# Performance work log

Hardware: AMD Instinct MI355X
Metric: run time of the kernel (lower is better)

## Reference

```python
import jax, jax.numpy as jnp
import numpy as np

UNITS = 1000


def gru_step(x, h, W, U, b):
    # Keras GRU, reset_after=True. b: [2, 3*units] = (input bias, recurrent bias)
    gx = x @ W + b[0]
    gh = h @ U + b[1]
    xz, xr, xh = jnp.split(gx, 3, axis=-1)
    hz, hr, hh_ = jnp.split(gh, 3, axis=-1)
    z = jax.nn.sigmoid(xz + hz)
    r = jax.nn.sigmoid(xr + hr)
    hh = jnp.tanh(xh + r * hh_)
    return z * h + (1.0 - z) * hh


def setup_inputs() -> dict:
    key = jax.random.key(0)
    ks = jax.random.split(key, 12)
    V1, E, U = 32001, 100, UNITS
    B, S = 64, 25
    sc = 0.05
    return {
        "x": jax.random.randint(ks[0], (B, S), 0, V1, dtype=jnp.int32),
        "target": jax.random.randint(ks[1], (B, S), 0, V1, dtype=jnp.int32),
        "start_token": 2,
        "emb_table": jax.random.normal(ks[2], (V1, E), jnp.float32) * sc,
        "enc_kernel": jax.random.normal(ks[3], (E, 3 * U), jnp.float32) * sc,
        "enc_recurrent": jax.random.normal(ks[4], (U, 3 * U), jnp.float32) * sc,
        "enc_bias": jax.random.normal(ks[5], (2, 3 * U), jnp.float32) * sc,
        "dec_kernel": jax.random.normal(ks[6], (E, 3 * U), jnp.float32) * sc,
        "dec_recurrent": jax.random.normal(ks[7], (U, 3 * U), jnp.float32) * sc,
        "dec_bias": jax.random.normal(ks[8], (2, 3 * U), jnp.float32) * sc,
        "fc_w": jax.random.normal(ks[9], (U, V1), jnp.float32) * sc,
        "fc_b": jnp.zeros((V1,), jnp.float32),
    }


def reference(x, target, start_token, emb_table, enc_kernel, enc_recurrent,
              enc_bias, dec_kernel, dec_recurrent, dec_bias, fc_w, fc_b):
    B, S = x.shape
    max_len = target.shape[1]

    # ---- Encoder (computed faithfully; its output is unused downstream,
    # matching the original where attention is never invoked) ----
    emb_x = emb_table[x]                      # [B,S,E]
    mask_x = (x != 0)                          # mask_zero embedding

    def enc_scan(h, xm):
        xt, mt = xm                            # xt:[B,E], mt:[B]
        hn = gru_step(xt, h, enc_kernel, enc_recurrent, enc_bias)
        h = jnp.where(mt[:, None], hn, h)      # masked steps carry state
        return h, h

    h0 = jnp.zeros((B, UNITS), emb_x.dtype)
    enc_state, enc_out = jax.lax.scan(
        enc_scan, h0, (jnp.swapaxes(emb_x, 0, 1), jnp.swapaxes(mask_x, 0, 1)))

    # ---- Decoder: original calls gru WITHOUT initial_state, so every step
    # starts from a zero hidden state -> all timesteps are independent. ----
    # teacher-forced inputs: [start_token, target[:, :-1]]
    tokens = jnp.concatenate(
        [jnp.full((B, 1), start_token, dtype=target.dtype), target[:, :-1]], axis=1)  # [B,T]
    emb_d = emb_table[tokens]                  # [B,T,E]
    mask_d = (tokens != 0)                     # [B,T]

    h_zero = jnp.zeros((B, max_len, UNITS), emb_d.dtype)
    h1 = gru_step(emb_d, h_zero, dec_kernel, dec_recurrent, dec_bias)  # [B,T,U]
    # masked single step -> output is the zero initial output
    h1 = jnp.where(mask_d[..., None], h1, 0.0)

    logits = h1 @ fc_w + fc_b                  # [B,T,V+1]
    app_emb = logits.astype(jnp.float32) @ emb_table  # [B,T,E]
    return app_emb
```

## Files before the change

kernel.cpp:

```cpp
#include <hip/hip_runtime.h>

typedef _Float16 half_t;
typedef _Float16 half8 __attribute__((ext_vector_type(8)));
typedef float    floatx4 __attribute__((ext_vector_type(4)));

#define V1     32001
#define EMBD   100
#define UNITS  1000
#define SEQ    25
#define NROWS  1600
#define HSTR   1024
#define NKB    63
#define UPQ    16
#define BROWS  128
#define BSTR   40

__global__ __launch_bounds__(256) void kPre(
    const float* __restrict__ E, half_t* __restrict__ ETu,
    const float* __restrict__ fcb, float* __restrict__ vvec,
    const int* __restrict__ target, const int* __restrict__ stok,
    const float* __restrict__ K, const float* __restrict__ bias,
    half_t* __restrict__ h1h)
{
    __shared__ char smem[100 * 66 * sizeof(half_t)];
    const int tid = threadIdx.x;
    const int bid = blockIdx.x;

    if (bid < 500) {
        half_t* lds = (half_t*)smem;
        const int k0 = bid * 64;
        const int e  = tid & 127;
        const int kh = tid >> 7;
        for (int kk = kh; kk < 64; kk += 2) {
            const int k = k0 + kk;
            if (e < 100) lds[e * 66 + kk] = (half_t)E[k * 100 + e];
        }
        __syncthreads();
        const int kl   = tid & 63;
        const int eh   = tid >> 6;
        const int unit = (k0 + kl) >> 5;
        const int kc   = kl & 31;
        half_t* dst = ETu + (long)unit * (BROWS * 32) + kc;
        for (int ee = eh; ee < BROWS; ee += 4)
            dst[ee * 32] = (ee < 100) ? lds[ee * 66 + kl] : (half_t)0.f;
        return;
    }

    if (bid < 756) {
        const int e  = tid & 127;
        const int g  = tid >> 7;
        const int ec = min(e, 99);
        const int slice = (bid - 500) * 2 + g;
        const int chunk = (V1 + 511) / 512;
        const int j0 = slice * chunk;
        const int j1 = min(j0 + chunk, V1);
        float acc = 0.f;
        for (int j = j0; j < j1; ++j)
            acc += fcb[j] * E[j * 100 + ec];
        if (e < 100) atomicAdd(&vvec[e], acc);
        return;
    }

    float (*xs)[100] = (float(*)[100])smem;
    __shared__ int msk[8];
    const int b3    = bid - 756;
    const int rg    = b3 % 200;
    const int uc    = b3 / 200;
    const int ibase = rg * 8;
    {
        const int r = tid >> 5, c = tid & 31;
        const int i = ibase + r;
        const int bb = i / SEQ, t = i - bb * SEQ;
        const int token = (t == 0) ? stok[0] : target[bb * SEQ + t - 1];
        if (c == 0) msk[r] = (token != 0);
        for (int cc = c; cc < 100; cc += 32)
            xs[r][cc] = E[token * 100 + cc];
    }
    __syncthreads();

    const int u = uc * 256 + tid;
    if (u < UNITS) {
        float az[8], ar[8], ah[8];
#pragma unroll
        for (int r = 0; r < 8; ++r) { az[r] = 0.f; ar[r] = 0.f; ah[r] = 0.f; }
#pragma unroll 4
        for (int k = 0; k < 100; ++k) {
            const float wz = K[k * 3000 + u];
            const float wr = K[k * 3000 + 1000 + u];
            const float wh = K[k * 3000 + 2000 + u];
#pragma unroll
            for (int r = 0; r < 8; ++r) {
                const float x = xs[r][k];
                az[r] += x * wz;
                ar[r] += x * wr;
                ah[r] += x * wh;
            }
        }
        const float* b0 = bias;
        const float* b1 = bias + 3000;
        const float bz  = b0[u] + b1[u];
        const float br  = b0[1000 + u] + b1[1000 + u];
        const float bh0 = b0[2000 + u];
        const float bh1 = b1[2000 + u];
#pragma unroll
        for (int r = 0; r < 8; ++r) {
            const float z   = 1.f / (1.f + __expf(-(az[r] + bz)));
            const float rg_ = 1.f / (1.f + __expf(-(ar[r] + br)));
            const float pre = ah[r] + bh0 + rg_ * bh1;
            const float ex  = __expf(2.f * pre);
            const float hh  = 1.f - 2.f / (ex + 1.f);
            h1h[(ibase + r) * HSTR + u] = (half_t)(msk[r] ? (1.f - z) * hh : 0.f);
        }
    } else {
        const half_t cv = (half_t)((u == 1000) ? 1.f : 0.f);
#pragma unroll
        for (int r = 0; r < 8; ++r)
            h1h[(ibase + r) * HSTR + u] = cv;
    }
}

__global__ __launch_bounds__(256) void kA(const float* __restrict__ W,
                                          const half_t* __restrict__ ETu,
                                          half_t* __restrict__ P)
{
    __shared__ half_t Bs[2][2][BROWS * BSTR];
    const int tid   = threadIdx.x;
    const int lane  = tid & 63;
    const int wv    = tid >> 6;
    const int mgrp  = blockIdx.x;
    const int kq    = blockIdx.y;
    const int row16 = lane & 15;
    const int quad  = lane >> 4;

    const int ub = kq * UPQ;
    const int nu = min(UPQ, UNITS - ub);
    const int np = nu >> 1;

    const int m  = mgrp * 64 + wv * 16 + row16;
    const int mc = min(m, UNITS - 1);
    const float* wrow = W + (long)mc * V1;

    const int srow  = tid >> 2;
    const int scol  = (tid & 3) * 8;
    const int soff0 = srow * BSTR + scol;
    const int soff1 = (64 + srow) * BSTR + scol;
    const int goff0 = tid * 8;
    const int goff1 = 2048 + tid * 8;

    floatx4 acc[7];
#pragma unroll
    for (int t = 0; t < 7; ++t) acc[t] = (floatx4){0.f, 0.f, 0.f, 0.f};

    half8 pb[4];
    float fa0[8], fa1[8];
    {
        const half_t* t0 = ETu + (long)ub * (BROWS * 32);
        pb[0] = *(const half8*)(t0 + goff0);
        pb[1] = *(const half8*)(t0 + goff1);
        pb[2] = *(const half8*)(t0 + BROWS * 32 + goff0);
        pb[3] = *(const half8*)(t0 + BROWS * 32 + goff1);
        __builtin_memcpy(fa0, wrow + ub * 32 + quad * 8, 32);
        __builtin_memcpy(fa1, wrow + (ub + 1) * 32 + quad * 8, 32);
    }

    for (int ip = 0; ip < np; ++ip) {
        *(half8*)(&Bs[ip & 1][0][soff0]) = pb[0];
        *(half8*)(&Bs[ip & 1][0][soff1]) = pb[1];
        *(half8*)(&Bs[ip & 1][1][soff0]) = pb[2];
        *(half8*)(&Bs[ip & 1][1][soff1]) = pb[3];
        half8 a0, a1;
#pragma unroll
        for (int q = 0; q < 8; ++q) { a0[q] = (half_t)fa0[q]; a1[q] = (half_t)fa1[q]; }
        if (ip + 1 < np) {
            const int u2 = ub + 2 * ip + 2;
            const half_t* nt = ETu + (long)u2 * (BROWS * 32);
            pb[0] = *(const half8*)(nt + goff0);
            pb[1] = *(const half8*)(nt + goff1);
            pb[2] = *(const half8*)(nt + BROWS * 32 + goff0);
            pb[3] = *(const half8*)(nt + BROWS * 32 + goff1);
            __builtin_memcpy(fa0, wrow + u2 * 32 + quad * 8, 32);
            __builtin_memcpy(fa1, wrow + (u2 + 1) * 32 + quad * 8, 32);
        }
        __syncthreads();
        const half_t* bp0 = &Bs[ip & 1][0][row16 * BSTR + quad * 8];
        const half_t* bp1 = &Bs[ip & 1][1][row16 * BSTR + quad * 8];
#pragma unroll
        for (int t = 0; t < 7; ++t) {
            const half8 b = *(const half8*)(bp0 + t * 16 * BSTR);
            acc[t] = __builtin_amdgcn_mfma_f32_16x16x32_f16(a0, b, acc[t], 0, 0, 0);
        }
#pragma unroll
        for (int t = 0; t < 7; ++t) {
            const half8 b = *(const half8*)(bp1 + t * 16 * BSTR);
            acc[t] = __builtin_amdgcn_mfma_f32_16x16x32_f16(a1, b, acc[t], 0, 0, 0);
        }
    }

    half_t* Pk = P + (long)kq * (1024 * 100);
    const int orow0 = mgrp * 64 + wv * 16 + quad * 4;
#pragma unroll
    for (int t = 0; t < 7; ++t) {
        const int col = t * 16 + row16;
        if (col < 100) {
#pragma unroll
            for (int r = 0; r < 4; ++r)
                Pk[(orow0 + r) * 100 + col] = (half_t)acc[t][r];
        }
    }
}

__global__ __launch_bounds__(256) void kPost(const half_t* __restrict__ P,
                                             const float* __restrict__ W,
                                             const float* __restrict__ E,
                                             const float* __restrict__ vvec,
                                             half_t* __restrict__ MbT)
{
    const int idx = blockIdx.x * 256 + threadIdx.x;
    const int kk  = idx / 100;
    const int e   = idx - kk * 100;
    float s;
    if (kk < 1000) {
        s = 0.f;
#pragma unroll 9
        for (int kb = 0; kb < NKB; ++kb)
            s += (float)P[(long)kb * (1024 * 100) + kk * 100 + e];
        s += W[(long)kk * V1 + 32000] * E[32000 * 100 + e];
    } else if (kk == 1000) {
        s = vvec[e];
    } else {
        s = 0.f;
    }
    MbT[e * HSTR + kk] = (half_t)s;
}

__global__ __launch_bounds__(256) void kC(const half_t* __restrict__ h1h,
                                          const half_t* __restrict__ MbT,
                                          float* __restrict__ out)
{
    __shared__ float red[3][64][29];
    const int tid   = threadIdx.x;
    const int lane  = tid & 63;
    const int wv    = tid >> 6;
    const int rb    = blockIdx.x;
    const int ks    = blockIdx.y;
    const int row16 = lane & 15;
    const int quad  = lane >> 4;

    const half_t* arow = h1h + (long)(rb * 16 + row16) * HSTR + quad * 8;
    const half_t* bbase[7];
#pragma unroll
    for (int t = 0; t < 7; ++t) {
        const int nc = min(t * 16 + row16, 99);
        bbase[t] = MbT + (long)nc * HSTR + quad * 8;
    }

    floatx4 acc[7];
#pragma unroll
    for (int t = 0; t < 7; ++t) acc[t] = (floatx4){0.f, 0.f, 0.f, 0.f};

    const int wb = ks * 8 + wv * 2;
#pragma unroll
    for (int un = wb; un < wb + 2; ++un) {
        const half8 a = *(const half8*)(arow + un * 32);
#pragma unroll
        for (int t = 0; t < 7; ++t) {
            const half8 b = *(const half8*)(bbase[t] + un * 32);
            acc[t] = __builtin_amdgcn_mfma_f32_16x16x32_f16(a, b, acc[t], 0, 0, 0);
        }
    }

    if (wv > 0) {
#pragma unroll
        for (int t = 0; t < 7; ++t)
#pragma unroll
            for (int r = 0; r < 4; ++r)
                red[wv - 1][lane][t * 4 + r] = acc[t][r];
    }
    __syncthreads();
    if (wv == 0) {
        const int orow0 = rb * 16 + quad * 4;
#pragma unroll
        for (int t = 0; t < 7; ++t) {
            const int col = t * 16 + row16;
            if (col < 100) {
#pragma unroll
                for (int r = 0; r < 4; ++r) {
                    const int i = t * 4 + r;
                    const float s = acc[t][r] + red[0][lane][i]
                                  + red[1][lane][i] + red[2][lane][i];
                    atomicAdd(&out[(orow0 + r) * 100 + col], s);
                }
            }
        }
    }
}

extern "C" void kernel_launch(void* const* d_in, const int* in_sizes, int n_in,
                              void* d_out, int out_size, void* d_ws, size_t ws_size,
                              hipStream_t stream)
{
    const int*   target     = (const int*)d_in[1];
    const int*   start_tok  = (const int*)d_in[2];
    const float* emb        = (const float*)d_in[3];
    const float* dec_kernel = (const float*)d_in[7];
    const float* dec_bias   = (const float*)d_in[9];
    const float* fc_w       = (const float*)d_in[10];
    const float* fc_b       = (const float*)d_in[11];

    float*  vvec = (float*)d_ws;
    half_t* ETu  = (half_t*)(vvec + 128);
    half_t* h1h  = ETu + (size_t)UNITS * (BROWS * 32);
    half_t* MbT  = h1h + (size_t)NROWS * HSTR;
    half_t* P    = MbT + (size_t)100 * HSTR;
    float*  out  = (float*)d_out;

    hipMemsetAsync(vvec, 0, 128 * sizeof(float), stream);
    hipMemsetAsync(out, 0, (size_t)NROWS * EMBD * sizeof(float), stream);

    kPre<<<1556, 256, 0, stream>>>(emb, ETu, fc_b, vvec, target, start_tok,
                                   dec_kernel, dec_bias, h1h);
    kA<<<dim3(16, NKB), 256, 0, stream>>>(fc_w, ETu, P);
    kPost<<<(1024 * 100) / 256, 256, 0, stream>>>(P, fc_w, emb, vvec, MbT);
    kC<<<dim3(100, 4), 256, 0, stream>>>(h1h, MbT, out);
}
```

Before: 293.5 us.

## Replace atomics with deterministic partial sums and drop memsets

The fc_b·E reduction now writes 64 per-slice partial vectors that kPost sums, instead of using atomicAdd into a zeroed buffer. kC is re-split so each block covers the full K range and half of the output columns, which lets it store results directly rather than atomically accumulating into a zeroed output. Both hipMemsetAsync calls are removed, saving two launches and the atomic traffic. In exchange, each kC block does more sequential K work, fewer kPre blocks share the bias reduction, and the tile loops use runtime bounds.

After: 393.1 us. 33.9% more time.

```diff
diff --git a/kernel.cpp b/kernel.cpp
--- a/kernel.cpp
+++ b/kernel.cpp
@@ -14,10 +14,11 @@
 #define UPQ    16
 #define BROWS  128
 #define BSTR   40
+#define VSLICE 64
 
 __global__ __launch_bounds__(256) void kPre(
     const float* __restrict__ E, half_t* __restrict__ ETu,
-    const float* __restrict__ fcb, float* __restrict__ vvec,
+    const float* __restrict__ fcb, float* __restrict__ vpart,
     const int* __restrict__ target, const int* __restrict__ stok,
     const float* __restrict__ K, const float* __restrict__ bias,
     half_t* __restrict__ h1h)
@@ -46,24 +47,23 @@
         return;
     }
 
-    if (bid < 756) {
+    if (bid < 532) {
         const int e  = tid & 127;
         const int g  = tid >> 7;
         const int ec = min(e, 99);
         const int slice = (bid - 500) * 2 + g;
-        const int chunk = (V1 + 511) / 512;
-        const int j0 = slice * chunk;
-        const int j1 = min(j0 + chunk, V1);
+        const int j0 = slice * 501;
+        const int j1 = min(j0 + 501, V1);
         float acc = 0.f;
         for (int j = j0; j < j1; ++j)
             acc += fcb[j] * E[j * 100 + ec];
-        if (e < 100) atomicAdd(&vvec[e], acc);
+        if (e < 100) vpart[slice * 100 + e] = acc;
         return;
     }
 
     float (*xs)[100] = (float(*)[100])smem;
     __shared__ int msk[8];
-    const int b3    = bid - 756;
+    const int b3    = bid - 532;
     const int rg    = b3 % 200;
     const int uc    = b3 / 200;
     const int ibase = rg * 8;
@@ -212,7 +212,7 @@
 __global__ __launch_bounds__(256) void kPost(const half_t* __restrict__ P,
                                              const float* __restrict__ W,
                                              const float* __restrict__ E,
-                                             const float* __restrict__ vvec,
+                                             const float* __restrict__ vpart,
                                              half_t* __restrict__ MbT)
 {
     const int idx = blockIdx.x * 256 + threadIdx.x;
@@ -226,7 +226,10 @@
             s += (float)P[(long)kb * (1024 * 100) + kk * 100 + e];
         s += W[(long)kk * V1 + 32000] * E[32000 * 100 + e];
     } else if (kk == 1000) {
-        s = vvec[e];
+        s = 0.f;
+#pragma unroll 8
+        for (int sl = 0; sl < VSLICE; ++sl)
+            s += vpart[sl * 100 + e];
     } else {
         s = 0.f;
     }
@@ -237,41 +240,41 @@
                                           const half_t* __restrict__ MbT,
                                           float* __restrict__ out)
 {
-    __shared__ float red[3][64][29];
+    __shared__ float red[3][64][17];
     const int tid   = threadIdx.x;
     const int lane  = tid & 63;
     const int wv    = tid >> 6;
     const int rb    = blockIdx.x;
-    const int ks    = blockIdx.y;
+    const int nh    = blockIdx.y;
     const int row16 = lane & 15;
     const int quad  = lane >> 4;
+    const int tbase = nh ? 4 : 0;
+    const int ntile = nh ? 3 : 4;
 
     const half_t* arow = h1h + (long)(rb * 16 + row16) * HSTR + quad * 8;
-    const half_t* bbase[7];
-#pragma unroll
-    for (int t = 0; t < 7; ++t) {
-        const int nc = min(t * 16 + row16, 99);
+    const half_t* bbase[4];
+#pragma unroll
+    for (int t = 0; t < 4; ++t) {
+        const int nc = min((tbase + t) * 16 + row16, 99);
         bbase[t] = MbT + (long)nc * HSTR + quad * 8;
     }
 
-    floatx4 acc[7];
-#pragma unroll
-    for (int t = 0; t < 7; ++t) acc[t] = (floatx4){0.f, 0.f, 0.f, 0.f};
-
-    const int wb = ks * 8 + wv * 2;
-#pragma unroll
-    for (int un = wb; un < wb + 2; ++un) {
+    floatx4 acc[4];
+#pragma unroll
+    for (int t = 0; t < 4; ++t) acc[t] = (floatx4){0.f, 0.f, 0.f, 0.f};
+
+    const int wb = wv * 8;
+#pragma unroll 2
+    for (int un = wb; un < wb + 8; ++un) {
         const half8 a = *(const half8*)(arow + un * 32);
-#pragma unroll
-        for (int t = 0; t < 7; ++t) {
+        for (int t = 0; t < ntile; ++t) {
             const half8 b = *(const half8*)(bbase[t] + un * 32);
             acc[t] = __builtin_amdgcn_mfma_f32_16x16x32_f16(a, b, acc[t], 0, 0, 0);
         }
     }
 
     if (wv > 0) {
-#pragma unroll
-        for (int t = 0; t < 7; ++t)
+        for (int t = 0; t < ntile; ++t)
 #pragma unroll
             for (int r = 0; r < 4; ++r)
                 red[wv - 1][lane][t * 4 + r] = acc[t][r];
@@ -279,16 +282,14 @@
     __syncthreads();
     if (wv == 0) {
         const int orow0 = rb * 16 + quad * 4;
-#pragma unroll
-        for (int t = 0; t < 7; ++t) {
-            const int col = t * 16 + row16;
+        for (int t = 0; t < ntile; ++t) {
+            const int col = (tbase + t) * 16 + row16;
             if (col < 100) {
 #pragma unroll
                 for (int r = 0; r < 4; ++r) {
                     const int i = t * 4 + r;
-                    const float s = acc[t][r] + red[0][lane][i]
-                                  + red[1][lane][i] + red[2][lane][i];
-                    atomicAdd(&out[(orow0 + r) * 100 + col], s);
+                    out[(orow0 + r) * 100 + col] = acc[t][r] + red[0][lane][i]
+                        + red[1][lane][i] + red[2][lane][i];
                 }
             }
         }
@@ -307,19 +308,16 @@
     const float* fc_w       = (const float*)d_in[10];
     const float* fc_b       = (const float*)d_in[11];
 
-    float*  vvec = (float*)d_ws;
-    half_t* ETu  = (half_t*)(vvec + 128);
-    half_t* h1h  = ETu + (size_t)UNITS * (BROWS * 32);
-    half_t* MbT  = h1h + (size_t)NROWS * HSTR;
-    half_t* P    = MbT + (size_t)100 * HSTR;
-    float*  out  = (float*)d_out;
-
-    hipMemsetAsync(vvec, 0, 128 * sizeof(float), stream);
-    hipMemsetAsync(out, 0, (size_t)NROWS * EMBD * sizeof(float), stream);
-
-    kPre<<<1556, 256, 0, stream>>>(emb, ETu, fc_b, vvec, target, start_tok,
+    float*  vpart = (float*)d_ws;
+    half_t* ETu   = (half_t*)(vpart + VSLICE * 100);
+    half_t* h1h   = ETu + (size_t)UNITS * (BROWS * 32);
+    half_t* MbT   = h1h + (size_t)NROWS * HSTR;
+    half_t* P     = MbT + (size_t)100 * HSTR;
+    float*  out   = (float*)d_out;
+
+    kPre<<<1332, 256, 0, stream>>>(emb, ETu, fc_b, vpart, target, start_tok,
                                    dec_kernel, dec_bias, h1h);
     kA<<<dim3(16, NKB), 256, 0, stream>>>(fc_w, ETu, P);
-    kPost<<<(1024 * 100) / 256, 256, 0, stream>>>(P, fc_w, emb, vvec, MbT);
-    kC<<<dim3(100, 4), 256, 0, stream>>>(h1h, MbT, out);
-}
+    kPost<<<(1024 * 100) / 256, 256, 0, stream>>>(P, fc_w, emb, vpart, MbT);
+    kC<<<dim3(100, 2), 256, 0, stream>>>(h1h, MbT, out);
+}
```
